# Kernel optimization log

Hardware: AMD Instinct MI355X
Metric: run time of the kernel (lower is better)

The kernel has to match this reference:

```python
import math
import jax, jax.numpy as jnp
import numpy as np

B, N, E, H, DH = 2, 1024, 512, 8, 64
KMAX, WIN = 8, 32
LOG_N = 11              # ceil(log2(max_seq_len+1)) for max_seq_len=1024
DP = LOG_N + 1          # depth-indexed parameter banks 0..log_n
LEVELS = 10             # log2(N): merge levels 1..10 (full binary tree over N leaves)
LN_EPS = 1e-5


def _build_static():
    """Static segment-tree layout: per-position causal cover sets + flat node slots."""
    leaf_start = 1 << LOG_N
    offs = [0]
    for d in range(LEVELS):
        offs.append(offs[-1] + (N >> d))
    M = offs[LEVELS] + 1  # levels 0..LEVELS, total 2N-1 nodes
    kvalid = np.ones(M, np.int32)
    for d in range(LEVELS + 1):
        kvalid[offs[d]:offs[d] + (N >> d)] = min(1 << d, KMAX)
    covers = []
    for pos in range(N):  # prefix [0..pos-1]
        l, r = leaf_start, leaf_start + pos
        out = []
        while l < r:
            if l & 1:
                out.append(l); l += 1
            if r & 1:
                r -= 1; out.append(r)
            l >>= 1; r >>= 1
        covers.append(out)
    S = max(1, max(len(c) for c in covers))
    ci = np.zeros((N, S), np.int32)
    cd = np.zeros((N, S), np.int32)
    cm = np.zeros((N, S), bool)
    for i, c in enumerate(covers):
        for s, node in enumerate(c):
            d = LOG_N - int(math.floor(math.log2(node)))
            ci[i, s] = offs[d] + (node - (leaf_start >> d))
            cd[i, s] = d
            cm[i, s] = True
    return ci, cd, cm, kvalid


def setup_inputs() -> dict:
    key = jax.random.key(0)
    ks = jax.random.split(key, 16)
    nrm = lambda k, s, sc=0.02: jax.random.normal(k, s, jnp.float32) * sc
    ci, cd, cm, kv = _build_static()
    return {
        "x": jax.random.normal(ks[0], (B, N, E), jnp.float32),
        "qW": nrm(ks[1], (E, E)), "qb": jnp.zeros((E,), jnp.float32),
        "vW": nrm(ks[2], (E, E)), "vb": jnp.zeros((E,), jnp.float32),
        "oW": nrm(ks[3], (E, E)), "ob": jnp.zeros((E,), jnp.float32),
        "klW": nrm(ks[4], (E, E)), "klb": jnp.zeros((E,), jnp.float32),
        "vlW": nrm(ks[5], (E, E)), "vlb": jnp.zeros((E,), jnp.float32),
        "gW": nrm(ks[6], (E, E)), "gb": jnp.full((E,), 2.0, jnp.float32),
        "ddqW": nrm(ks[7], (DP, DH, DH)),
        "ddqT": jnp.linspace(0.5, 4.0, DP).astype(jnp.float32),
        "wfreq": jnp.linspace(0.3, 4.0, H).astype(jnp.float32),
        "wdamp": jnp.linspace(-3.0, 0.5, H).astype(jnp.float32),
        "wphase": jnp.linspace(0.0, math.pi, H).astype(jnp.float32),
        "glW": nrm(ks[8], (DP, DH, 2 * DH)), "glb": jnp.full((DP, DH), 0.5, jnp.float32),
        "grW": nrm(ks[9], (DP, DH, 2 * DH)), "grb": jnp.full((DP, DH), 0.5, jnp.float32),
        "pq": nrm(ks[10], (DP, KMAX, DH)),
        "lnG": jnp.ones((DP, DH), jnp.float32), "lnB": jnp.zeros((DP, DH), jnp.float32),
        "skA": jnp.full((DP,), 0.1, jnp.float32),
        "skW": nrm(ks[11], (DP, DH, DH)),
        "coup": jnp.eye(H, dtype=jnp.float32)[None] + nrm(ks[12], (DP, H, H), 0.01),
        "cov_idx": jnp.asarray(ci), "cov_depth": jnp.asarray(cd),
        "cov_mask": jnp.asarray(cm), "kvalid": jnp.asarray(kv),
    }


def reference(x, qW, qb, vW, vb, oW, ob, klW, klb, vlW, vlb, gW, gb, ddqW, ddqT,
              wfreq, wdamp, wphase, glW, glb, grW, grb, pq, lnG, lnB, skA, skW,
              coup, cov_idx, cov_depth, cov_mask, kvalid):
    q = (x @ qW.T + qb).reshape(B, N, H, DH)
    v = (x @ vW.T + vb).reshape(B, N, H, DH)

    # ---- local exact causal window attention ----
    k_loc = (x @ klW.T + klb).reshape(B, N, H, DH)
    v_loc = (x @ vlW.T + vlb).reshape(B, N, H, DH)
    j = jnp.arange(N)[:, None] - jnp.arange(WIN)[None, :]  # (N, W) key positions
    valid = j >= 0
    jc = jnp.clip(j, 0, N - 1)
    kg = k_loc[:, jc]  # (B,N,W,H,DH)
    vg = v_loc[:, jc]
    sc = jnp.einsum('bnhd,bnwhd->bhnw', q, kg) / math.sqrt(DH)
    sc = jnp.where(valid[None, None], sc, -1e9)
    local = jnp.einsum('bhnw,bnwhd->bnhd', jax.nn.softmax(sc, axis=-1), vg)

    # ---- build segment tree, vectorized per depth level ----
    alpha_b = jax.nn.softplus(wdamp)
    cur = jnp.transpose(v, (0, 2, 1, 3))[:, :, :, None, :]  # leaves (B,H,N,1,DH)
    levels = [cur]
    for d in range(1, LEVELS + 1):
        fL, fR = cur[:, :, 0::2], cur[:, :, 1::2]  # (B,H,n,K,DH)
        # depth-scaled complex rotation (alpha_d*dt = alpha, omega_d*dt = omega)
        scale = float(1 << (LOG_N - d))
        dec = jnp.exp(-(alpha_b / scale) * scale)
        ang = (wfreq / scale) * scale + (wphase + d * (math.pi / 4.0))
        pr = (dec * jnp.cos(ang)).reshape(1, H, 1, 1, 1)
        pi_ = (dec * jnp.sin(ang)).reshape(1, H, 1, 1, 1)
        d2 = DH // 2
        fre, fim = fR[..., :d2], fR[..., d2:]
        rot = jnp.concatenate([pr * fre - pi_ * fim, pi_ * fre + pr * fim], -1)
        lm, rm = fL.mean(3), rot.mean(3)  # (B,H,n,DH)
        gin = jnp.concatenate([lm, rm], -1)
        gl = jax.nn.sigmoid(gin @ glW[d].T + glb[d])[..., None, :]
        gr = jax.nn.sigmoid(gin @ grW[d].T + grb[d])[..., None, :]
        bank = jnp.concatenate([fL * gl, rot * gr], 3)  # (B,H,n,2K,DH)
        kp = min(2 * cur.shape[3], KMAX)
        att = jax.nn.softmax(
            jnp.einsum('qd,bhnkd->bhnqk', pq[d, :kp], bank) / math.sqrt(DH), -1)
        par = jnp.einsum('bhnqk,bhnkd->bhnqd', att, bank)
        mu = par.mean(-1, keepdims=True)
        par = (par - mu) * jax.lax.rsqrt(par.var(-1, keepdims=True) + LN_EPS)
        par = par * lnG[d] + lnB[d]
        par = par + jax.nn.sigmoid(skA[d]) * (lm @ skW[d].T)[..., None, :]
        cur = jnp.einsum('ij,bjnkd->binkd', jax.nn.softmax(coup[d], -1), par)
        levels.append(cur)

    # flat node bank padded to KMAX vectors per node: (B,H,M,KMAX,DH)
    bank_all = jnp.concatenate(
        [jnp.pad(lv, ((0, 0), (0, 0), (0, 0), (0, KMAX - lv.shape[3]), (0, 0)))
         for lv in levels], axis=2)

    # ---- depth-decomposed query over causal cover sets ----
    Qall = q[None] + jnp.einsum('bnhd,ped->pbnhe', q, ddqW)  # (DP,B,N,H,DH)
    sc_d = 1.0 / ((jax.nn.softplus(ddqT) + 1e-6) * math.sqrt(DH))
    Qt = jnp.transpose(Qall, (2, 0, 1, 3, 4))  # (N,DP,B,H,DH)
    Qg = Qt[jnp.arange(N)[:, None], cov_depth]  # (N,S,B,H,DH)
    bg = bank_all[:, :, cov_idx]  # (B,H,N,S,KMAX,DH)
    scores = jnp.einsum('nsbhd,bhnskd->bhnsk', Qg, bg)
    scores = scores * sc_d[cov_depth][None, None, :, :, None]
    kmsk = jnp.arange(KMAX)[None, None] < kvalid[cov_idx][:, :, None]
    msk = cov_mask[:, :, None] & kmsk  # (N,S,KMAX)
    scores = jnp.where(msk[None, None], scores, -1e9)
    aw = jax.nn.softmax(scores.reshape(B, H, N, -1), -1).reshape(scores.shape)
    tree_out = jnp.einsum('bhnsk,bhnskd->bnhd', aw, bg)
    tree_out = jnp.where(cov_mask.any(1)[None, :, None, None], tree_out, 0.0)

    gate = jax.nn.sigmoid(x @ gW.T + gb).reshape(B, N, H, DH)
    out = (local + gate * tree_out).reshape(B, N, E)
    return out @ oW.T + ob
```

## Files before the change

### kernel.cpp

```cpp
#include <hip/hip_runtime.h>
#include <math.h>

#define B_ 2
#define N_ 1024
#define H_ 8
#define TOTV 5104

typedef __attribute__((ext_vector_type(8))) short bf16x8;
typedef __attribute__((ext_vector_type(4))) float f32x4;

__device__ __constant__ int VBASE[11] = {0,1024,2048,3072,4096,4608,4864,4992,5056,5088,5104};

constexpr int vbase_of(int d) {
  int v = 0;
  for (int i = 0; i < d; ++i) v += (1024 >> i) * ((i >= 3) ? 8 : (1 << i));
  return v;
}

__device__ __forceinline__ float wsum(float v) {
  v += __shfl_xor(v, 1);  v += __shfl_xor(v, 2);  v += __shfl_xor(v, 4);
  v += __shfl_xor(v, 8);  v += __shfl_xor(v, 16); v += __shfl_xor(v, 32);
  return v;
}
__device__ __forceinline__ float sigmoidf_(float x) { return 1.f / (1.f + __expf(-x)); }
__device__ __forceinline__ unsigned short f2b(float f) {
  unsigned u = __float_as_uint(f);
  return (unsigned short)((u + 0x7FFFu + ((u >> 16) & 1u)) >> 16);
}
__device__ __forceinline__ float b2f(unsigned short h) {
  return __uint_as_float(((unsigned)h) << 16);
}
__device__ __forceinline__ float dot4(float4 a, float4 b) {
  return a.x*b.x + a.y*b.y + a.z*b.z + a.w*b.w;
}
__device__ __forceinline__ float rl(float v, int l) {
  return __uint_as_float(__builtin_amdgcn_readlane(__float_as_uint(v), l));
}

__global__ void prep_kernel(const float* __restrict__ x,
                            const float* __restrict__ w0, const float* __restrict__ w1,
                            const float* __restrict__ w2, const float* __restrict__ w3,
                            const float* __restrict__ w4, const float* __restrict__ oW,
                            const float* __restrict__ ddqW, const float* __restrict__ ddqT,
                            unsigned short* __restrict__ A2x, unsigned short* __restrict__ B2w,
                            unsigned short* __restrict__ B2o, unsigned short* __restrict__ B2q)
{
  const int bx = blockIdx.x;
  const int tid = threadIdx.x;
  if (bx < 1024) {
    int i = (bx * 256 + tid) * 4;
    int m = i >> 9, k = i & 511;
    float4 f = *(const float4*)(x + i);
    float fv[4] = {f.x, f.y, f.z, f.w};
    unsigned short h[4], l[4];
#pragma unroll
    for (int j = 0; j < 4; ++j) { h[j] = f2b(fv[j]); l[j] = f2b(fv[j] - b2f(h[j])); }
    size_t base = (size_t)m * 1536;
    ushort4 hv = {h[0], h[1], h[2], h[3]};
    ushort4 lv = {l[0], l[1], l[2], l[3]};
    *(ushort4*)(A2x + base + k) = hv;
    *(ushort4*)(A2x + base + 512 + k) = lv;
    *(ushort4*)(A2x + base + 1024 + k) = hv;
  } else if (bx < 2304) {
    int i = ((bx - 1024) * 256 + tid) * 4;
    int nrow = i >> 9, k = i & 511;
    int sel = nrow >> 9;
    const float* w = sel == 0 ? w0 : sel == 1 ? w1 : sel == 2 ? w2 : sel == 3 ? w3 : w4;
    float4 f = *(const float4*)(w + (size_t)(nrow & 511) * 512 + k);
    float fv[4] = {f.x, f.y, f.z, f.w};
    unsigned short h[4], l[4];
#pragma unroll
    for (int j = 0; j < 4; ++j) { h[j] = f2b(fv[j]); l[j] = f2b(fv[j] - b2f(h[j])); }
    size_t base = (size_t)nrow * 1536;
    ushort4 hv = {h[0], h[1], h[2], h[3]};
    ushort4 lv = {l[0], l[1], l[2], l[3]};
    *(ushort4*)(B2w + base + k) = hv;
    *(ushort4*)(B2w + base + 512 + k) = hv;
    *(ushort4*)(B2w + base + 1024 + k) = lv;
  } else if (bx < 2560) {
    int i = ((bx - 2304) * 256 + tid) * 4;
    int m = i >> 9, k = i & 511;
    float4 f = *(const float4*)(oW + i);
    float fv[4] = {f.x, f.y, f.z, f.w};
    unsigned short h[4], l[4];
#pragma unroll
    for (int j = 0; j < 4; ++j) { h[j] = f2b(fv[j]); l[j] = f2b(fv[j] - b2f(h[j])); }
    size_t base = (size_t)m * 1536;
    ushort4 hv = {h[0], h[1], h[2], h[3]};
    ushort4 lv = {l[0], l[1], l[2], l[3]};
    *(ushort4*)(B2o + base + k) = hv;
    *(ushort4*)(B2o + base + 512 + k) = hv;
    *(ushort4*)(B2o + base + 1024 + k) = lv;
  } else {
    int i = (bx - 2560) * 256 + tid;
    int row = i >> 6, e = i & 63;
    int p = row >> 6, o = row & 63;
    float t = ddqT[p];
    float sp = log1pf(__expf(t));
    float scd = 1.f / ((sp + 1e-6f) * 8.0f);
    float w = (ddqW[(size_t)(p * 64 + o) * 64 + e] + (o == e ? 1.f : 0.f)) * scd;
    unsigned short h = f2b(w);
    unsigned short l = f2b(w - b2f(h));
    size_t base = (size_t)row * 192;
    B2q[base + e] = h; B2q[base + 64 + e] = h; B2q[base + 128 + e] = l;
  }
}

template<int MODE>
__global__ __launch_bounds__(256)
void gemm_mfma(const unsigned short* __restrict__ A2, const unsigned short* __restrict__ B2,
               int K3,
               const float* __restrict__ bq, const float* __restrict__ bv,
               const float* __restrict__ bkl, const float* __restrict__ bvl,
               const float* __restrict__ bgt,
               float* __restrict__ qbuf, float* __restrict__ bank,
               float* __restrict__ klbuf, float* __restrict__ vlbuf,
               float* __restrict__ gatebuf, float* __restrict__ Qs,
               float* __restrict__ oout, const float* __restrict__ ob,
               unsigned short* __restrict__ A2q)
{
  __shared__ __align__(16) unsigned short Asb[128 * 40];
  __shared__ __align__(16) unsigned short Bsb[128 * 40];
  const int tid = threadIdx.x;
  const int wave = tid >> 6, lane = tid & 63;
  const int wr = wave >> 1, wc = wave & 1;
  const int row0 = blockIdx.y * 128, col0 = blockIdx.x * 128;

  f32x4 acc[4][4];
#pragma unroll
  for (int i = 0; i < 4; ++i)
#pragma unroll
    for (int j = 0; j < 4; ++j) acc[i][j] = (f32x4){0.f, 0.f, 0.f, 0.f};

  const int srow = tid >> 1;
  const int shalf = tid & 1;
  const unsigned short* agp = A2 + (size_t)(row0 + srow) * K3 + shalf * 16;
  const unsigned short* bgp = B2 + (size_t)(col0 + srow) * K3 + shalf * 16;
  const int lrow = lane & 15, kslot = lane >> 4;

  for (int kt = 0; kt < K3; kt += 32) {
    int4 a0 = *(const int4*)(agp + kt);
    int4 a1 = *(const int4*)(agp + kt + 8);
    int4 b0 = *(const int4*)(bgp + kt);
    int4 b1 = *(const int4*)(bgp + kt + 8);
    __syncthreads();
    *(int4*)(Asb + srow * 40 + shalf * 16) = a0;
    *(int4*)(Asb + srow * 40 + shalf * 16 + 8) = a1;
    *(int4*)(Bsb + srow * 40 + shalf * 16) = b0;
    *(int4*)(Bsb + srow * 40 + shalf * 16 + 8) = b1;
    __syncthreads();
    bf16x8 af[4], bf[4];
#pragma unroll
    for (int m = 0; m < 4; ++m)
      af[m] = *(const bf16x8*)(Asb + (wr * 64 + m * 16 + lrow) * 40 + kslot * 8);
#pragma unroll
    for (int n = 0; n < 4; ++n)
      bf[n] = *(const bf16x8*)(Bsb + (wc * 64 + n * 16 + lrow) * 40 + kslot * 8);
#pragma unroll
    for (int m = 0; m < 4; ++m)
#pragma unroll
      for (int n = 0; n < 4; ++n)
        acc[m][n] = __builtin_amdgcn_mfma_f32_16x16x32_bf16(af[m], bf[n], acc[m][n], 0, 0, 0);
  }

#pragma unroll
  for (int m = 0; m < 4; ++m)
#pragma unroll
    for (int n = 0; n < 4; ++n)
#pragma unroll
      for (int r = 0; r < 4; ++r) {
        const int row = row0 + wr * 64 + m * 16 + (lane >> 4) * 4 + r;
        const int col = col0 + wc * 64 + n * 16 + (lane & 15);
        float v = acc[m][n][r];
        if (MODE == 0) {
          const int sel = col >> 9;
          const int c = col & 511;
          const int bb = row >> 10, nn = row & 1023;
          if (sel == 0) {
            float vv = v + bq[c];
            qbuf[(size_t)row * 512 + c] = vv;
            unsigned short hi = f2b(vv), lo = f2b(vv - b2f(hi));
            size_t mq = (size_t)row * 8 + (c >> 6);
            int kq = c & 63;
            A2q[mq * 192 + kq] = hi;
            A2q[mq * 192 + 64 + kq] = lo;
            A2q[mq * 192 + 128 + kq] = hi;
          } else if (sel == 1) {
            bank[((size_t)(bb * 8 + (c >> 6)) * TOTV + nn) * 64 + (c & 63)] = v + bv[c];
          } else if (sel == 2) {
            klbuf[(size_t)row * 512 + c] = v + bkl[c];
          } else if (sel == 3) {
            vlbuf[(size_t)row * 512 + c] = v + bvl[c];
          } else {
            gatebuf[(size_t)row * 512 + c] = sigmoidf_(v + bgt[c]);
          }
        } else if (MODE == 1) {
          Qs[((size_t)(col >> 6) * 16384 + row) * 64 + (col & 63)] = v;
        } else {
          oout[(size_t)row * 512 + col] = v + ob[col];
        }
      }
}

template<int D, int NPB>
__global__ __launch_bounds__(512)
void level5(const float* __restrict__ glW, const float* __restrict__ glb,
            const float* __restrict__ grW, const float* __restrict__ grb,
            const float* __restrict__ pq, const float* __restrict__ lnG,
            const float* __restrict__ lnB, const float* __restrict__ skA,
            const float* __restrict__ skW, const float* __restrict__ coup,
            const float* __restrict__ wfreq, const float* __restrict__ wdamp,
            const float* __restrict__ wphase, float* __restrict__ bank)
{
  constexpr int KPREV = ((D - 1) >= 3) ? 8 : (1 << (D - 1));
  constexpr int SLOTS = 2 * KPREV;
  constexpr int KP = (D >= 3) ? 8 : (1 << D);
  constexpr bool TP = (D >= 3);
  constexpr int VB_PREV = vbase_of(D - 1);
  constexpr int VB_CUR  = vbase_of(D);

  __shared__ __align__(8)  float wpk[128 * 130];
  __shared__ float sklds[64 * 65];
  __shared__ float parlds[8][KP][64];
  __shared__ __align__(16) float slds[TP ? 8 * SLOTS * 68 : 1];
  __shared__ float wlds[TP ? 8 * KP * 17 : 1];
  __shared__ __align__(16) float pqlds[TP ? KP * 68 : 1];

  const int tid = threadIdx.x;
  const int h = tid >> 6, lane = tid & 63;
  const int b = blockIdx.y;

  for (int i = tid; i < 64 * 128; i += 512) {
    int o = i >> 7, e = i & 127;
    wpk[e * 130 + 2 * o]     = glW[(size_t)D * 8192 + i];
    wpk[e * 130 + 2 * o + 1] = grW[(size_t)D * 8192 + i];
  }
  for (int i = tid; i < 64 * 64; i += 512) {
    int o = i >> 6, e = i & 63;
    sklds[e * 65 + o] = skW[(size_t)D * 4096 + i];
  }
  if constexpr (TP) {
    for (int i = tid; i < KP * 64; i += 512)
      pqlds[(i >> 6) * 68 + (i & 63)] = pq[(size_t)D * 512 + i];
  }
  __syncthreads();

  const float alpha = log1pf(__expf(wdamp[h]));
  const float dec = __expf(-alpha);
  const float ang = wfreq[h] + wphase[h] + (float)D * 0.78539816339744831f;
  const float pr  = dec * cosf(ang);
  const float pim = dec * sinf(ang);
  const float glbv = glb[D * 64 + lane], grbv = grb[D * 64 + lane];
  const float lnGv = lnG[D * 64 + lane], lnBv = lnB[D * 64 + lane];
  const float sig_sk = sigmoidf_(skA[D]);
  float cw[8];
  float cmx = -1e30f;
#pragma unroll
  for (int j = 0; j < 8; ++j) { cw[j] = coup[(size_t)(D * 8 + h) * 8 + j]; cmx = fmaxf(cmx, cw[j]); }
  float cs = 0.f;
#pragma unroll
  for (int j = 0; j < 8; ++j) { cw[j] = __expf(cw[j] - cmx); cs += cw[j]; }
  const float cinv = 1.f / cs;

  const size_t bh = (size_t)(b * H_ + h);
  const float* prevb = bank + (bh * TOTV + VB_PREV) * 64;
  float* curb = bank + (bh * TOTV + VB_CUR) * 64;

  for (int nn = 0; nn < NPB; ++nn) {
    const int node = blockIdx.x * NPB + nn;
    float par[KP];
    float fL[KPREV], rot[KPREV];
    {
      float lm = 0.f, rm = 0.f;
#pragma unroll
      for (int k = 0; k < KPREV; ++k) {
        fL[k] = prevb[(size_t)((2 * node) * KPREV + k) * 64 + lane];
        float fr = prevb[(size_t)((2 * node + 1) * KPREV + k) * 64 + lane];
        float partner = __shfl_xor(fr, 32);
        rot[k] = (lane < 32) ? (pr * fr - pim * partner) : (pim * partner + pr * fr);
        lm += fL[k]; rm += rot[k];
      }
      lm *= (1.f / KPREV); rm *= (1.f / KPREV);

      float gl = glbv, gr = grbv, sk = 0.f;
#pragma unroll
      for (int e = 0; e < 64; ++e) {
        float g = rl(lm, e);
        float2 w2 = *(const float2*)&wpk[e * 130 + 2 * lane];
        gl += g * w2.x;
        gr += g * w2.y;
        sk += g * sklds[e * 65 + lane];
      }
#pragma unroll
      for (int e = 0; e < 64; ++e) {
        float g = rl(rm, e);
        float2 w2 = *(const float2*)&wpk[(64 + e) * 130 + 2 * lane];
        gl += g * w2.x;
        gr += g * w2.y;
      }
      gl = sigmoidf_(gl); gr = sigmoidf_(gr);

      float slot[SLOTS];
#pragma unroll
      for (int k = 0; k < KPREV; ++k) { slot[k] = fL[k] * gl; slot[KPREV + k] = rot[k] * gr; }

      if constexpr (!TP) {
        float pqv[KP];
#pragma unroll
        for (int qi = 0; qi < KP; ++qi) pqv[qi] = pq[(size_t)(D * 8 + qi) * 64 + lane];
#pragma unroll
        for (int qi = 0; qi < KP; ++qi) {
          float lg[SLOTS];
          float mx = -1e30f;
#pragma unroll
          for (int kk = 0; kk < SLOTS; ++kk) {
            lg[kk] = wsum(pqv[qi] * slot[kk]) * 0.125f;
            mx = fmaxf(mx, lg[kk]);
          }
          float den = 0.f, pv = 0.f;
#pragma unroll
          for (int kk = 0; kk < SLOTS; ++kk) {
            float w = __expf(lg[kk] - mx);
            den += w; pv += w * slot[kk];
          }
          par[qi] = pv / den;
        }
      } else {
        float* sl = &slds[h * SLOTS * 68];
#pragma unroll
        for (int kk = 0; kk < SLOTS; ++kk) sl[kk * 68 + lane] = slot[kk];
        constexpr int PAIRS = KP * SLOTS;
        const int kk0 = lane & (SLOTS - 1);
        const int qg  = lane / SLOTS;
        float s0 = 0.f, s1 = 0.f;
        {
          const float4* sv = (const float4*)&sl[kk0 * 68];
          const float4* q0 = (const float4*)&pqlds[qg * 68];
#pragma unroll
          for (int e = 0; e < 16; ++e) s0 += dot4(q0[e], sv[e]);
          if constexpr (PAIRS == 128) {
            const float4* q1 = (const float4*)&pqlds[(qg + 4) * 68];
#pragma unroll
            for (int e = 0; e < 16; ++e) s1 += dot4(q1[e], sv[e]);
          }
        }
        s0 *= 0.125f; s1 *= 0.125f;
        float m0 = s0, m1 = s1;
#pragma unroll
        for (int o = 1; o < SLOTS; o <<= 1) {
          m0 = fmaxf(m0, __shfl_xor(m0, o));
          if constexpr (PAIRS == 128) m1 = fmaxf(m1, __shfl_xor(m1, o));
        }
        float e0 = __expf(s0 - m0), e1 = (PAIRS == 128) ? __expf(s1 - m1) : 0.f;
        float d0 = e0, d1 = e1;
#pragma unroll
        for (int o = 1; o < SLOTS; o <<= 1) {
          d0 += __shfl_xor(d0, o);
          if constexpr (PAIRS == 128) d1 += __shfl_xor(d1, o);
        }
        float* wld = &wlds[h * KP * 17];
        wld[qg * 17 + kk0] = e0 / d0;
        if constexpr (PAIRS == 128) wld[(qg + 4) * 17 + kk0] = e1 / d1;
#pragma unroll
        for (int qi = 0; qi < KP; ++qi) {
          float acc2 = 0.f;
#pragma unroll
          for (int kk = 0; kk < SLOTS; ++kk) acc2 += wld[qi * 17 + kk] * slot[kk];
          par[qi] = acc2;
        }
      }

#pragma unroll
      for (int qi = 0; qi < KP; ++qi) {
        float mu = wsum(par[qi]) * (1.f / 64.f);
        float dv = par[qi] - mu;
        float var = wsum(dv * dv) * (1.f / 64.f);
        float nv = dv * rsqrtf(var + 1e-5f);
        par[qi] = nv * lnGv + lnBv + sig_sk * sk;
        parlds[h][qi][lane] = par[qi];
      }
    }
    __syncthreads();
#pragma unroll
    for (int qi = 0; qi < KP; ++qi) {
      float o = 0.f;
#pragma unroll
      for (int j = 0; j < 8; ++j) o += cw[j] * parlds[j][qi][lane];
      curb[(size_t)(node * KP + qi) * 64 + lane] = o * cinv;
    }
    __syncthreads();
  }
}

__global__ __launch_bounds__(512)
void combine3(const float* __restrict__ qbuf, const float* __restrict__ klbuf,
              const float* __restrict__ vlbuf, const float* __restrict__ gatebuf,
              const float* __restrict__ bank, const float* __restrict__ Qs,
              unsigned short* __restrict__ A2o)
{
  const int flat = blockIdx.y * 1024 + blockIdx.x;
  const int swz = (flat & 7) * 256 + (flat >> 3);
  const int n = swz & 1023;
  const int b = swz >> 10;
  const int h = threadIdx.x >> 6;
  const int lane = threadIdx.x & 63;
  __shared__ int pair_ro[64];
  __shared__ int pair_sl[64];
  __shared__ int sdepth[16];
  __shared__ int PS[2];
  __shared__ __align__(16) float Qlds[8][10][68];
  __shared__ __align__(16) float qlds[8][64];
  __shared__ float sclds[8][64];

  if (threadIdx.x == 0) {
    int l = 2048, r = 2048 + n;
    int cnt = 0, sc = 0;
    while (l < r) {
      if (l & 1) {
        int m = l++;
        int j = 31 - __clz(m);
        int d = 11 - j;
        int local = m - (1 << j);
        int kv = (d >= 3) ? 8 : (1 << d);
        sdepth[sc] = d;
        int vb = VBASE[d] + local * kv;
        for (int k = 0; k < kv; ++k) { pair_ro[cnt] = (vb + k) * 64; pair_sl[cnt] = sc; ++cnt; }
        ++sc;
      }
      if (r & 1) {
        int m = --r;
        int j = 31 - __clz(m);
        int d = 11 - j;
        int local = m - (1 << j);
        int kv = (d >= 3) ? 8 : (1 << d);
        sdepth[sc] = d;
        int vb = VBASE[d] + local * kv;
        for (int k = 0; k < kv; ++k) { pair_ro[cnt] = (vb + k) * 64; pair_sl[cnt] = sc; ++cnt; }
        ++sc;
      }
      l >>= 1; r >>= 1;
    }
    PS[0] = cnt; PS[1] = sc;
    for (int k = cnt; k < 64; ++k) { pair_ro[k] = 0; pair_sl[k] = 0; }
  }
  const size_t vbase = ((size_t)(b * N_ + n) * H_ + h) * 64;
  qlds[h][lane] = qbuf[vbase + lane];
  __syncthreads();
  const int P = PS[0], S = PS[1];

  for (int s = 0; s < S; ++s)
    Qlds[h][s][lane] = Qs[((size_t)sdepth[s] * 16384 + (size_t)(b * N_ + n) * H_ + h) * 64 + lane];

  const int w = lane & 31, half = lane >> 5;
  const int wmax = (n + 1 < 32) ? (n + 1) : 32;
  float scl = 0.f;
  if (w < wmax) {
    const float4* k4 = (const float4*)(klbuf + vbase - (size_t)w * 512 + half * 32);
    const float4* q4 = (const float4*)&qlds[h][half * 32];
#pragma unroll
    for (int e = 0; e < 8; ++e) scl += dot4(q4[e], k4[e]);
  }
  scl += __shfl_xor(scl, 32);
  scl *= 0.125f;
  float sm = (w < wmax) ? scl : -1e30f;
  float mx = sm;
#pragma unroll
  for (int o = 1; o < 32; o <<= 1) mx = fmaxf(mx, __shfl_xor(mx, o));
  float le = (w < wmax) ? __expf(sm - mx) : 0.f;
  float den = le;
#pragma unroll
  for (int o = 1; o < 32; o <<= 1) den += __shfl_xor(den, o);
  float lp = le / den;
  float local = 0.f;
  if (n >= 31) {
#pragma unroll 8
    for (int ww = 0; ww < 32; ++ww) {
      float pw = __shfl(lp, ww);
      local += pw * vlbuf[vbase - (size_t)ww * 512 + lane];
    }
  } else {
    for (int ww = 0; ww < wmax; ++ww) {
      float pw = __shfl(lp, ww);
      local += pw * vlbuf[vbase - (size_t)ww * 512 + lane];
    }
  }

  const size_t bhbase = (size_t)(b * H_ + h) * TOTV * 64;
  float tree = 0.f;
  if (P > 0) {
    const int passes = (P + 15) >> 4;
    for (int t = 0; t < passes; ++t) {
      const int p = (t << 4) + (lane >> 2);
      const int c = lane & 3;
      float s = 0.f;
      if (p < P) {
        const float4* b4 = (const float4*)(bank + bhbase + pair_ro[p] + c * 16);
        const float4* q4 = (const float4*)&Qlds[h][pair_sl[p]][c * 16];
#pragma unroll
        for (int i = 0; i < 4; ++i) s += dot4(q4[i], b4[i]);
      }
      s += __shfl_xor(s, 1);
      s += __shfl_xor(s, 2);
      if (c == 0 && p < P) sclds[h][p] = s;
    }
    float logit = (lane < P) ? sclds[h][lane] : -1e30f;
    float tm = logit;
#pragma unroll
    for (int o = 1; o < 64; o <<= 1) tm = fmaxf(tm, __shfl_xor(tm, o));
    float te = (lane < P) ? __expf(logit - tm) : 0.f;
    float tden = te;
#pragma unroll
    for (int o = 1; o < 64; o <<= 1) tden += __shfl_xor(tden, o);
    float tw = te / tden;
    const int P4 = (P + 3) & ~3;
    for (int l2 = 0; l2 < P4; l2 += 4) {
      float w0_ = __shfl(tw, l2),     w1_ = __shfl(tw, l2 + 1);
      float w2_ = __shfl(tw, l2 + 2), w3_ = __shfl(tw, l2 + 3);
      float v0 = bank[bhbase + pair_ro[l2]     + lane];
      float v1 = bank[bhbase + pair_ro[l2 + 1] + lane];
      float v2 = bank[bhbase + pair_ro[l2 + 2] + lane];
      float v3 = bank[bhbase + pair_ro[l2 + 3] + lane];
      tree += w0_ * v0 + w1_ * v1 + w2_ * v2 + w3_ * v3;
    }
  }

  float g = gatebuf[vbase + lane];
  float v = local + g * tree;
  unsigned short hi = f2b(v), lo = f2b(v - b2f(hi));
  const size_t m = (size_t)(b * N_ + n);
  const int k = h * 64 + lane;
  A2o[m * 1536 + k] = hi;
  A2o[m * 1536 + 512 + k] = lo;
  A2o[m * 1536 + 1024 + k] = hi;
}

extern "C" void kernel_launch(void* const* d_in, const int* in_sizes, int n_in,
                              void* d_out, int out_size, void* d_ws, size_t ws_size,
                              hipStream_t stream)
{
  (void)in_sizes; (void)n_in; (void)out_size; (void)ws_size;
  const float* x     = (const float*)d_in[0];
  const float* qW    = (const float*)d_in[1];
  const float* qb    = (const float*)d_in[2];
  const float* vW    = (const float*)d_in[3];
  const float* vb    = (const float*)d_in[4];
  const float* oW    = (const float*)d_in[5];
  const float* ob    = (const float*)d_in[6];
  const float* klW   = (const float*)d_in[7];
  const float* klb   = (const float*)d_in[8];
  const float* vlW   = (const float*)d_in[9];
  const float* vlb   = (const float*)d_in[10];
  const float* gW    = (const float*)d_in[11];
  const float* gb    = (const float*)d_in[12];
  const float* ddqW  = (const float*)d_in[13];
  const float* ddqT  = (const float*)d_in[14];
  const float* wfreq = (const float*)d_in[15];
  const float* wdamp = (const float*)d_in[16];
  const float* wphase= (const float*)d_in[17];
  const float* glW   = (const float*)d_in[18];
  const float* glb   = (const float*)d_in[19];
  const float* grW   = (const float*)d_in[20];
  const float* grb   = (const float*)d_in[21];
  const float* pq    = (const float*)d_in[22];
  const float* lnG   = (const float*)d_in[23];
  const float* lnB   = (const float*)d_in[24];
  const float* skA   = (const float*)d_in[25];
  const float* skW   = (const float*)d_in[26];
  const float* coup  = (const float*)d_in[27];

  float* ws = (float*)d_ws;
  float* qbuf    = ws; ws += (size_t)2048 * 512;
  float* klbuf   = ws; ws += (size_t)2048 * 512;
  float* vlbuf   = ws; ws += (size_t)2048 * 512;
  float* gatebuf = ws; ws += (size_t)2048 * 512;
  float* bank    = ws; ws += (size_t)16 * TOTV * 64;
  float* Qs      = ws; ws += (size_t)10 * 16384 * 64;
  unsigned short* A2x = (unsigned short*)ws; ws += (size_t)2048 * 1536 / 2;
  unsigned short* B2w = (unsigned short*)ws; ws += (size_t)2560 * 1536 / 2;
  unsigned short* A2q = (unsigned short*)ws; ws += (size_t)16384 * 192 / 2;
  unsigned short* B2q = (unsigned short*)ws; ws += (size_t)640 * 192 / 2;
  unsigned short* A2o = (unsigned short*)ws; ws += (size_t)2048 * 1536 / 2;
  unsigned short* B2o = (unsigned short*)ws; ws += (size_t)512 * 1536 / 2;

  prep_kernel<<<2720, 256, 0, stream>>>(x, qW, vW, klW, vlW, gW, oW, ddqW, ddqT,
                                        A2x, B2w, B2o, B2q);

  gemm_mfma<0><<<dim3(20, 16), 256, 0, stream>>>(A2x, B2w, 1536,
      qb, vb, klb, vlb, gb, qbuf, bank, klbuf, vlbuf, gatebuf,
      nullptr, nullptr, nullptr, A2q);

  gemm_mfma<1><<<dim3(5, 128), 256, 0, stream>>>(A2q, B2q, 192,
      nullptr, nullptr, nullptr, nullptr, nullptr,
      nullptr, nullptr, nullptr, nullptr, nullptr, Qs, nullptr, nullptr, nullptr);

#define LVL(DD, NPB) level5<DD, NPB><<<dim3((1024 >> DD) / NPB, 2), 512, 0, stream>>>( \
      glW, glb, grW, grb, pq, lnG, lnB, skA, skW, coup, wfreq, wdamp, wphase, bank)
  LVL(1, 4); LVL(2, 2); LVL(3, 1); LVL(4, 1); LVL(5, 1);
  LVL(6, 1); LVL(7, 1); LVL(8, 1); LVL(9, 1);
#undef LVL

  combine3<<<dim3(1024, 2), 512, 0, stream>>>(qbuf, klbuf, vlbuf, gatebuf, bank, Qs, A2o);

  gemm_mfma<2><<<dim3(4, 16), 256, 0, stream>>>(A2o, B2o, 1536,
      nullptr, nullptr, nullptr, nullptr, nullptr,
      nullptr, nullptr, nullptr, nullptr, nullptr, nullptr,
      (float*)d_out, ob, nullptr);
}
```

Baseline: 426.2 us.

## Load GEMM tiles directly to LDS with swizzle and shrink tile width

The GEMM kernel now uses global_load_lds to move A/B tiles straight from global memory into LDS, skipping the register staging, and uses an XOR swizzle instead of padding to avoid bank conflicts. Tile N shrinks from 128 to 64, and M is templated (128 or 64), so grids double or quadruple for better CU occupancy on the small GEMMs. Each tile now gets less data reuse and issues fewer MFMAs per sync, and there is still no double buffering.

```diff
diff --git a/kernel.cpp b/kernel.cpp
--- a/kernel.cpp
+++ b/kernel.cpp
@@ -35,6 +35,11 @@
 }
 __device__ __forceinline__ float rl(float v, int l) {
   return __uint_as_float(__builtin_amdgcn_readlane(__float_as_uint(v), l));
+}
+__device__ __forceinline__ void gl16(const unsigned short* g, unsigned short* l) {
+  __builtin_amdgcn_global_load_lds(
+      (const __attribute__((address_space(1))) unsigned int*)g,
+      (__attribute__((address_space(3))) unsigned int*)l, 16, 0, 0);
 }
 
 __global__ void prep_kernel(const float* __restrict__ x,
@@ -106,10 +111,10 @@
   }
 }
 
-template<int MODE>
+template<int MODE, int BM>
 __global__ __launch_bounds__(256)
 void gemm_mfma(const unsigned short* __restrict__ A2, const unsigned short* __restrict__ B2,
-               int K3,
+               const int K3,
                const float* __restrict__ bq, const float* __restrict__ bv,
                const float* __restrict__ bkl, const float* __restrict__ bvl,
                const float* __restrict__ bgt,
@@ -119,58 +124,68 @@
                float* __restrict__ oout, const float* __restrict__ ob,
                unsigned short* __restrict__ A2q)
 {
-  __shared__ __align__(16) unsigned short Asb[128 * 40];
-  __shared__ __align__(16) unsigned short Bsb[128 * 40];
+  constexpr int MREP = BM / 32;
+  __shared__ __align__(16) unsigned short Alds[BM * 32];
+  __shared__ __align__(16) unsigned short Blds[64 * 32];
   const int tid = threadIdx.x;
   const int wave = tid >> 6, lane = tid & 63;
   const int wr = wave >> 1, wc = wave & 1;
-  const int row0 = blockIdx.y * 128, col0 = blockIdx.x * 128;
-
-  f32x4 acc[4][4];
-#pragma unroll
-  for (int i = 0; i < 4; ++i)
-#pragma unroll
-    for (int j = 0; j < 4; ++j) acc[i][j] = (f32x4){0.f, 0.f, 0.f, 0.f};
-
-  const int srow = tid >> 1;
-  const int shalf = tid & 1;
-  const unsigned short* agp = A2 + (size_t)(row0 + srow) * K3 + shalf * 16;
-  const unsigned short* bgp = B2 + (size_t)(col0 + srow) * K3 + shalf * 16;
+  const int row0 = blockIdx.y * BM, col0 = blockIdx.x * 64;
+
+  f32x4 acc[MREP][2];
+#pragma unroll
+  for (int i = 0; i < MREP; ++i)
+#pragma unroll
+    for (int j = 0; j < 2; ++j) acc[i][j] = (f32x4){0.f, 0.f, 0.f, 0.f};
+
+  const int rIn = lane >> 2;
+  const int jIn = lane & 3;
+  const int arow0 = (BM == 128 ? (2 * wave) * 16 : wave * 16) + rIn;
+  const int arow1 = (2 * wave + 1) * 16 + rIn;
+  const int brow  = wave * 16 + rIn;
+  const unsigned short* aSrc0 = A2 + (size_t)(row0 + arow0) * K3 + ((jIn ^ ((arow0 >> 1) & 3)) << 3);
+  const unsigned short* aSrc1 = A2 + (size_t)(row0 + (BM == 128 ? arow1 : arow0)) * K3
+                                   + ((jIn ^ (((BM == 128 ? arow1 : arow0) >> 1) & 3)) << 3);
+  const unsigned short* bSrc  = B2 + (size_t)(col0 + brow) * K3 + ((jIn ^ ((brow >> 1) & 3)) << 3);
+  unsigned short* aDst0 = Alds + (BM == 128 ? (2 * wave) * 512 : wave * 512);
+  unsigned short* aDst1 = Alds + (BM == 128 ? (2 * wave + 1) * 512 : wave * 512);
+  unsigned short* bDst  = Blds + wave * 512;
+
   const int lrow = lane & 15, kslot = lane >> 4;
 
   for (int kt = 0; kt < K3; kt += 32) {
-    int4 a0 = *(const int4*)(agp + kt);
-    int4 a1 = *(const int4*)(agp + kt + 8);
-    int4 b0 = *(const int4*)(bgp + kt);
-    int4 b1 = *(const int4*)(bgp + kt + 8);
     __syncthreads();
-    *(int4*)(Asb + srow * 40 + shalf * 16) = a0;
-    *(int4*)(Asb + srow * 40 + shalf * 16 + 8) = a1;
-    *(int4*)(Bsb + srow * 40 + shalf * 16) = b0;
-    *(int4*)(Bsb + srow * 40 + shalf * 16 + 8) = b1;
+    gl16(aSrc0 + kt, aDst0);
+    if constexpr (BM == 128) gl16(aSrc1 + kt, aDst1);
+    gl16(bSrc + kt, bDst);
     __syncthreads();
-    bf16x8 af[4], bf[4];
-#pragma unroll
-    for (int m = 0; m < 4; ++m)
-      af[m] = *(const bf16x8*)(Asb + (wr * 64 + m * 16 + lrow) * 40 + kslot * 8);
-#pragma unroll
-    for (int n = 0; n < 4; ++n)
-      bf[n] = *(const bf16x8*)(Bsb + (wc * 64 + n * 16 + lrow) * 40 + kslot * 8);
-#pragma unroll
-    for (int m = 0; m < 4; ++m)
-#pragma unroll
-      for (int n = 0; n < 4; ++n)
+
+    bf16x8 af[MREP], bf[2];
+#pragma unroll
+    for (int m = 0; m < MREP; ++m) {
+      const int r = wr * (BM / 2) + m * 16 + lrow;
+      af[m] = *(const bf16x8*)(Alds + r * 32 + ((kslot ^ ((r >> 1) & 3)) << 3));
+    }
+#pragma unroll
+    for (int n = 0; n < 2; ++n) {
+      const int r = wc * 32 + n * 16 + lrow;
+      bf[n] = *(const bf16x8*)(Blds + r * 32 + ((kslot ^ ((r >> 1) & 3)) << 3));
+    }
+#pragma unroll
+    for (int m = 0; m < MREP; ++m)
+#pragma unroll
+      for (int n = 0; n < 2; ++n)
         acc[m][n] = __builtin_amdgcn_mfma_f32_16x16x32_bf16(af[m], bf[n], acc[m][n], 0, 0, 0);
   }
 
 #pragma unroll
-  for (int m = 0; m < 4; ++m)
-#pragma unroll
-    for (int n = 0; n < 4; ++n)
+  for (int m = 0; m < MREP; ++m)
+#pragma unroll
+    for (int n = 0; n < 2; ++n)
 #pragma unroll
       for (int r = 0; r < 4; ++r) {
-        const int row = row0 + wr * 64 + m * 16 + (lane >> 4) * 4 + r;
-        const int col = col0 + wc * 64 + n * 16 + (lane & 15);
+        const int row = row0 + wr * (BM / 2) + m * 16 + (lane >> 4) * 4 + r;
+        const int col = col0 + wc * 32 + n * 16 + (lane & 15);
         float v = acc[m][n][r];
         if (MODE == 0) {
           const int sel = col >> 9;
@@ -585,11 +600,11 @@
   prep_kernel<<<2720, 256, 0, stream>>>(x, qW, vW, klW, vlW, gW, oW, ddqW, ddqT,
                                         A2x, B2w, B2o, B2q);
 
-  gemm_mfma<0><<<dim3(20, 16), 256, 0, stream>>>(A2x, B2w, 1536,
+  gemm_mfma<0, 128><<<dim3(40, 16), 256, 0, stream>>>(A2x, B2w, 1536,
       qb, vb, klb, vlb, gb, qbuf, bank, klbuf, vlbuf, gatebuf,
       nullptr, nullptr, nullptr, A2q);
 
-  gemm_mfma<1><<<dim3(5, 128), 256, 0, stream>>>(A2q, B2q, 192,
+  gemm_mfma<1, 128><<<dim3(10, 128), 256, 0, stream>>>(A2q, B2q, 192,
       nullptr, nullptr, nullptr, nullptr, nullptr,
       nullptr, nullptr, nullptr, nullptr, nullptr, Qs, nullptr, nullptr, nullptr);
 
@@ -601,7 +616,7 @@
 
   combine3<<<dim3(1024, 2), 512, 0, stream>>>(qbuf, klbuf, vlbuf, gatebuf, bank, Qs, A2o);
 
-  gemm_mfma<2><<<dim3(4, 16), 256, 0, stream>>>(A2o, B2o, 1536,
+  gemm_mfma<2, 64><<<dim3(8, 32), 256, 0, stream>>>(A2o, B2o, 1536,
       nullptr, nullptr, nullptr, nullptr, nullptr,
       nullptr, nullptr, nullptr, nullptr, nullptr, nullptr,
       (float*)d_out, ob, nullptr);
```

Result: faster. 388.2 us (-8.9%).
